# Optimization experiments

Hardware: AMD Instinct MI355X
Metric: run time of the kernel (lower is better)

Reference implementation:

```python
import jax, jax.numpy as jnp
import numpy as np

VOCAB, EMBD, H1, H2, OUT = 100000, 128, 256, 128, 1
EPS = 1e-12

def _layernorm(x, g, b):
    mu = jnp.mean(x, axis=-1, keepdims=True)
    var = jnp.mean(jnp.square(x - mu), axis=-1, keepdims=True)
    return (x - mu) * jax.lax.rsqrt(var + EPS) * g + b

def setup_inputs() -> dict:
    key = jax.random.key(0)
    ks = jax.random.split(key, 10)
    B, S = 4096, 50
    return {
        "entity_ids": jax.random.randint(ks[0], (B, S), 0, VOCAB),
        "entity_length": jax.random.randint(ks[1], (B,), 0, S + 1),
        "emb_table": jax.random.normal(ks[2], (VOCAB, EMBD), jnp.float32),
        "ln1_g": jnp.ones((EMBD,), jnp.float32),
        "ln1_b": jnp.zeros((EMBD,), jnp.float32),
        "w1": jax.random.normal(ks[3], (EMBD, H1), jnp.float32) * (1.0 / np.sqrt(EMBD)),
        "b1": jnp.zeros((H1,), jnp.float32),
        "w2": jax.random.normal(ks[4], (H1, H2), jnp.float32) * (1.0 / np.sqrt(H1)),
        "b2": jnp.zeros((H2,), jnp.float32),
        "ln2_g": jnp.ones((H2,), jnp.float32),
        "ln2_b": jnp.zeros((H2,), jnp.float32),
        "fc_w": jax.random.normal(ks[5], (H2, OUT), jnp.float32) * (1.0 / np.sqrt(H2)),
        "fc_b": jnp.zeros((OUT,), jnp.float32),
    }

def reference(entity_ids, entity_length, emb_table, ln1_g, ln1_b, w1, b1, w2, b2, ln2_g, ln2_b, fc_w, fc_b):
    # embed: [B, S, EMBD]
    x = emb_table[entity_ids]
    x = _layernorm(x, ln1_g, ln1_b)
    # MLP (dropout is identity in eval); torch GELU default is exact erf form
    x = jax.nn.gelu(x @ w1 + b1, approximate=False) @ w2 + b2  # [B, S, H2]
    # ragged max-pool over first length positions (length 0 treated as 1)
    lengths = jnp.maximum(entity_length, 1)  # [B]
    S = x.shape[1]
    mask = jnp.arange(S)[None, :] < lengths[:, None]  # [B, S]
    x = jnp.max(jnp.where(mask[:, :, None], x, -jnp.inf), axis=1)  # [B, H2]
    x = _layernorm(x, ln2_g, ln2_b)
    return (x @ fc_w + fc_b).squeeze(-1)  # [B]
```

## Files before the change

kernel.cpp:

```cpp
#include <hip/hip_runtime.h>
#include <hip/hip_bf16.h>
#include <math.h>

typedef __attribute__((ext_vector_type(8))) _Float16 half8;
typedef __attribute__((ext_vector_type(4))) _Float16 half4;
typedef __attribute__((ext_vector_type(4))) float f32x4;

#define EMBD 128
#define H1 256
#define H2 128
#define SLEN 50
#define NROWS 4096
#define MTILE 32
#define DENSE_GRID 512

#define WS_FRAGS   0
#define WS_CNT     131072
#define WS_PACKED  131200
#define WS_PARTIAL 950400

__device__ __forceinline__ float gelu_exact(float h) {
    float ah = fabsf(h);
    float d  = fmaf(0.23163845f, ah, 1.0f);
    float t;
    asm("v_rcp_f32 %0, %1" : "=v"(t) : "v"(d));
    float p = fmaf(1.061405429f, t, -1.453152027f);
    p = fmaf(p, t, 1.421413741f);
    p = fmaf(p, t, -0.284496736f);
    p = fmaf(p, t, 0.254829592f);
    p = p * t;
    float e;
    float x2 = h * h * -0.72134752f;
    asm("v_exp_f32 %0, %1" : "=v"(e) : "v"(x2));
    float er = fmaf(-p, e, 1.0f);
    return fmaf(0.5f * ah, er, 0.5f * h);
}

#define BARRIER_LDS() asm volatile("s_waitcnt lgkmcnt(0)\n\ts_barrier" ::: "memory")

__global__ __launch_bounds__(256) void setup_kernel(
    const float* __restrict__ w1, const float* __restrict__ w2,
    const int* __restrict__ ids, const int* __restrict__ lens,
    half8* __restrict__ frags, unsigned* __restrict__ packed,
    int* __restrict__ cnt, float* __restrict__ partial)
{
    int b = blockIdx.x, t = threadIdx.x;
    if (b < 32) {
        int f = b * 256 + t;
        half8 v;
        if (f < 4096) {
            int fragid = f >> 6, lane = f & 63;
            int kt = fragid >> 4, nt = fragid & 15;
            int col = nt * 16 + (lane & 15);
            int kb  = kt * 32 + (lane >> 4) * 8;
            #pragma unroll
            for (int i = 0; i < 8; ++i) v[i] = (_Float16)w1[(size_t)(kb + i) * H1 + col];
            frags[f] = v;
        } else {
            int f2 = f - 4096;
            int fragid = f2 >> 6, lane = f2 & 63;
            int kt = fragid >> 3, ntc = fragid & 7;
            int col = ntc * 16 + (lane & 15);
            int kb  = kt * 32 + (lane >> 4) * 8;
            #pragma unroll
            for (int i = 0; i < 8; ++i) v[i] = (_Float16)w2[(size_t)(kb + i) * H2 + col];
            frags[4096 + f2] = v;
        }
    } else if (b < 48) {
        int gtid = (b - 32) * 256 + t;
        int lane = t & 63;
        int len = lens[gtid]; len = len < 1 ? 1 : (len > SLEN ? SLEN : len);
        int inc = len;
        #pragma unroll
        for (int off = 1; off < 64; off <<= 1) {
            int v = __shfl_up(inc, off, 64);
            if (lane >= off) inc += v;
        }
        int wave_total = __shfl(inc, 63, 64);
        int wbase;
        if (lane == 0) wbase = atomicAdd(cnt, wave_total);
        wbase = __shfl(wbase, 0, 64);
        int base = wbase + inc - len;
        unsigned rtag = (unsigned)gtid << 17;
        for (int k = 0; k < len; ++k)
            packed[base + k] = (unsigned)ids[gtid * SLEN + k] | rtag;
    } else {
        float4 ninf = { -INFINITY, -INFINITY, -INFINITY, -INFINITY };
        float4* p4 = (float4*)partial;
        int idx = (b - 48) * 256 + t;
        for (int e = idx; e < NROWS * 64; e += 64 * 256) {
            int row = e >> 6, rem = e & 63;
            p4[row * 96 + 32 + rem] = ninf;
        }
    }
}

__global__ __launch_bounds__(512) void dense_kernel(
    const unsigned* __restrict__ packed, const int* __restrict__ cnt,
    const float* __restrict__ emb, const float* __restrict__ ln1g,
    const float* __restrict__ ln1b, const float* __restrict__ b1,
    const float* __restrict__ b2, const half8* __restrict__ wfrag,
    float* __restrict__ partial)
{
    const int tid = threadIdx.x;
    const int w  = tid >> 6;
    const int l  = tid & 63;
    const int ln = l & 15;
    const int lg = l >> 4;
    const int g32 = w * 4 + lg;

    __shared__ __align__(16) _Float16 x_lds[MTILE][EMBD + 8];
    __shared__ __align__(16) _Float16 h1_lds[MTILE][H1 + 8];
    __shared__ unsigned tok_lds[MTILE + 1];
    __shared__ __align__(16) float b1s[H1];
    __shared__ float b2s[H2];

    if (tid < H1) b1s[tid] = b1[tid];
    else if (tid < H1 + H2) b2s[tid - H1] = b2[tid - H1];

    half8 w1r[4][2];
    #pragma unroll
    for (int kt = 0; kt < 4; ++kt)
      #pragma unroll
      for (int j = 0; j < 2; ++j)
        w1r[kt][j] = wfrag[(kt * 16 + w * 2 + j) * 64 + l];
    half8 w2r[8];
    #pragma unroll
    for (int kt = 0; kt < 8; ++kt)
        w2r[kt] = wfrag[4096 + (kt * 8 + w) * 64 + l];

    float g1r[8], b1r[8];
    #pragma unroll
    for (int i = 0; i < 8; ++i) { g1r[i] = ln1g[ln * 8 + i]; b1r[i] = ln1b[ln * 8 + i]; }

    const int total = *cnt;

    int tile = blockIdx.x;
    int base = tile * MTILE;

    unsigned pkA = 0xFFFFFFFFu, tokA = 0xFFFFFFFFu;
    float4 pa0, pa1; bool vA = false;
    if (base < total) {
        if (base + g32 < total) pkA = packed[base + g32];
        if (tid <= 32) {
            int ti = (tid < 32) ? base + tid : base - 1;
            tokA = (ti >= 0 && ti < total) ? packed[ti] : 0xFFFFFFFFu;
        }
        vA = (pkA != 0xFFFFFFFFu);
        if (vA) {
            const float4* src = (const float4*)(emb + (size_t)(pkA & 0x1FFFFu) * EMBD + ln * 8);
            pa0 = src[0]; pa1 = src[1];
        }
    }

    for (; base < total; tile += (int)gridDim.x, base = tile * MTILE) {
        const int nbase = (tile + (int)gridDim.x) * MTILE;

        if (tid <= 32) tok_lds[tid] = tokA;

        unsigned pkN = 0xFFFFFFFFu, tokN = 0xFFFFFFFFu;
        if (nbase < total) {
            if (nbase + g32 < total) pkN = packed[nbase + g32];
            if (tid <= 32) {
                int ti = (tid < 32) ? nbase + tid : nbase - 1;
                tokN = (ti < total) ? packed[ti] : 0xFFFFFFFFu;
            }
        }

        {
            half8 xo;
            if (vA) {
                float v[8] = {pa0.x, pa0.y, pa0.z, pa0.w, pa1.x, pa1.y, pa1.z, pa1.w};
                float sm = 0.f, ss = 0.f;
                #pragma unroll
                for (int k = 0; k < 8; ++k) { sm += v[k]; ss += v[k] * v[k]; }
                #pragma unroll
                for (int m = 1; m < 16; m <<= 1) {
                    sm += __shfl_xor(sm, m, 64);
                    ss += __shfl_xor(ss, m, 64);
                }
                float mu  = sm * (1.f / 128.f);
                float var = ss * (1.f / 128.f) - mu * mu;
                float rs  = rsqrtf(var + 1e-12f);
                #pragma unroll
                for (int k = 0; k < 8; ++k)
                    xo[k] = (_Float16)((v[k] - mu) * rs * g1r[k] + b1r[k]);
            } else {
                #pragma unroll
                for (int k = 0; k < 8; ++k) xo[k] = (_Float16)0.f;
            }
            *(half8*)&x_lds[g32][ln * 8] = xo;
        }

        BARRIER_LDS();

        f32x4 acc[2][2];
        acc[0][0] = (f32x4){0,0,0,0}; acc[0][1] = (f32x4){0,0,0,0};
        acc[1][0] = (f32x4){0,0,0,0}; acc[1][1] = (f32x4){0,0,0,0};
        #pragma unroll
        for (int kt = 0; kt < 4; ++kt) {
            half8 xf0 = *(const half8*)&x_lds[ln][kt * 32 + lg * 8];
            half8 xf1 = *(const half8*)&x_lds[16 + ln][kt * 32 + lg * 8];
            acc[0][0] = __builtin_amdgcn_mfma_f32_16x16x32_f16(w1r[kt][0], xf0, acc[0][0], 0, 0, 0);
            acc[0][1] = __builtin_amdgcn_mfma_f32_16x16x32_f16(w1r[kt][1], xf0, acc[0][1], 0, 0, 0);
            acc[1][0] = __builtin_amdgcn_mfma_f32_16x16x32_f16(w1r[kt][0], xf1, acc[1][0], 0, 0, 0);
            acc[1][1] = __builtin_amdgcn_mfma_f32_16x16x32_f16(w1r[kt][1], xf1, acc[1][1], 0, 0, 0);
        }

        float4 pb0, pb1; bool vN = (pkN != 0xFFFFFFFFu);
        if (vN) {
            const float4* src = (const float4*)(emb + (size_t)(pkN & 0x1FFFFu) * EMBD + ln * 8);
            pb0 = src[0]; pb1 = src[1];
        }

        #pragma unroll
        for (int m = 0; m < 2; ++m)
          #pragma unroll
          for (int j = 0; j < 2; ++j) {
            f32x4 bb = *(const f32x4*)&b1s[(w * 2 + j) * 16 + lg * 4];
            half4 hv;
            #pragma unroll
            for (int g2 = 0; g2 < 4; ++g2) {
                float h = acc[m][j][g2] + bb[g2];
                hv[g2] = (_Float16)gelu_exact(h);
            }
            *(half4*)&h1_lds[m * 16 + ln][(w * 2 + j) * 16 + lg * 4] = hv;
          }

        int rowj = 0x7FFF, rowp = 0x7FFF;
        if (l < 32) {
            rowj = (int)(tok_lds[l] >> 17);
            rowp = (l == 0) ? (int)(tok_lds[32] >> 17) : (int)(tok_lds[l - 1] >> 17);
        }
        const int prevrow = (int)(tok_lds[32] >> 17);
        bool st = (l < 32) && ((l == 0) || (rowj != rowp));
        unsigned mask = (unsigned)__ballot(st);
        const float b2v = b2s[w * 16 + ln];

        BARRIER_LDS();

        f32x4 acc2[2];
        acc2[0] = (f32x4){0,0,0,0}; acc2[1] = (f32x4){0,0,0,0};
        #pragma unroll
        for (int kt = 0; kt < 8; ++kt) {
            half8 a0 = *(const half8*)&h1_lds[ln][kt * 32 + lg * 8];
            half8 a1 = *(const half8*)&h1_lds[16 + ln][kt * 32 + lg * 8];
            acc2[0] = __builtin_amdgcn_mfma_f32_16x16x32_f16(a0, w2r[kt], acc2[0], 0, 0, 0);
            acc2[1] = __builtin_amdgcn_mfma_f32_16x16x32_f16(a1, w2r[kt], acc2[1], 0, 0, 0);
        }
        float val[2][4];
        #pragma unroll
        for (int m = 0; m < 2; ++m)
          #pragma unroll
          for (int g2 = 0; g2 < 4; ++g2)
            val[m][g2] = acc2[m][g2] + b2v;

        {
            int s0 = 0;
            while (s0 < 32) {
                int s1;
                if (s0 >= 31) s1 = 32;
                else {
                    unsigned m2 = mask >> (s0 + 1);
                    s1 = m2 ? (s0 + __ffs(m2)) : 32;
                }
                int row = __shfl(rowj, s0, 64);
                if (row < NROWS) {
                    float mx = -INFINITY;
                    #pragma unroll
                    for (int m = 0; m < 2; ++m)
                      #pragma unroll
                      for (int g2 = 0; g2 < 4; ++g2) {
                        int tt = m * 16 + lg * 4 + g2;
                        if (tt >= s0 && tt < s1) mx = fmaxf(mx, val[m][g2]);
                      }
                    mx = fmaxf(mx, __shfl_xor(mx, 16, 64));
                    mx = fmaxf(mx, __shfl_xor(mx, 32, 64));
                    int side = (s0 == 0 && row == prevrow) ? 1 + (tile & 1) : 0;
                    if (l < 16)
                        partial[(size_t)row * 384 + side * 128 + w * 16 + l] = mx;
                }
                s0 = s1;
            }
        }

        pkA = pkN; tokA = tokN; vA = vN;
        if (vN) { pa0 = pb0; pa1 = pb1; }
    }
}

__global__ __launch_bounds__(256) void head_kernel(
    const float* __restrict__ partial, const float* __restrict__ ln2g,
    const float* __restrict__ ln2b, const float* __restrict__ fcw,
    const float* __restrict__ fcb, float* __restrict__ out)
{
    int w = threadIdx.x >> 6, l = threadIdx.x & 63;
    int r = blockIdx.x * 4 + w;
    const float* pr = partial + (size_t)r * 384;
    float v0 = fmaxf(fmaxf(pr[l],      pr[128 + l]),      pr[256 + l]);
    float v1 = fmaxf(fmaxf(pr[64 + l], pr[128 + 64 + l]), pr[256 + 64 + l]);
    float g2a = ln2g[l], g2c = ln2g[l + 64];
    float b2a = ln2b[l], b2c = ln2b[l + 64];
    float fwa = fcw[l],  fwc = fcw[l + 64];
    float s = v0 + v1, ss = v0 * v0 + v1 * v1;
    #pragma unroll
    for (int m = 1; m < 64; m <<= 1) {
        s  += __shfl_xor(s,  m, 64);
        ss += __shfl_xor(ss, m, 64);
    }
    float mu  = s * (1.f / 128.f);
    float var = ss * (1.f / 128.f) - mu * mu;
    float rs  = rsqrtf(var + 1e-12f);
    float n0 = (v0 - mu) * rs * g2a + b2a;
    float n1 = (v1 - mu) * rs * g2c + b2c;
    float dot = n0 * fwa + n1 * fwc;
    #pragma unroll
    for (int m = 1; m < 64; m <<= 1) dot += __shfl_xor(dot, m, 64);
    if (l == 0) out[r] = dot + fcb[0];
}

extern "C" void kernel_launch(void* const* d_in, const int* in_sizes, int n_in,
                              void* d_out, int out_size, void* d_ws, size_t ws_size,
                              hipStream_t stream) {
    const int*   ids  = (const int*)d_in[0];
    const int*   lens = (const int*)d_in[1];
    const float* emb  = (const float*)d_in[2];
    const float* ln1g = (const float*)d_in[3];
    const float* ln1b = (const float*)d_in[4];
    const float* w1   = (const float*)d_in[5];
    const float* b1   = (const float*)d_in[6];
    const float* w2   = (const float*)d_in[7];
    const float* b2   = (const float*)d_in[8];
    const float* ln2g = (const float*)d_in[9];
    const float* ln2b = (const float*)d_in[10];
    const float* fcw  = (const float*)d_in[11];
    const float* fcb  = (const float*)d_in[12];
    float* out = (float*)d_out;

    char* ws = (char*)d_ws;
    half8*    frags   = (half8*)(ws + WS_FRAGS);
    int*      cnt     = (int*)(ws + WS_CNT);
    unsigned* packed  = (unsigned*)(ws + WS_PACKED);
    float*    partial = (float*)(ws + WS_PARTIAL);

    hipMemsetAsync(cnt, 0, sizeof(int), stream);
    hipLaunchKernelGGL(setup_kernel, dim3(112), dim3(256), 0, stream,
                       w1, w2, ids, lens, frags, packed, cnt, partial);
    hipLaunchKernelGGL(dense_kernel, dim3(DENSE_GRID), dim3(512), 0, stream,
                       packed, cnt, emb, ln1g, ln1b, b1, b2, frags, partial);
    hipLaunchKernelGGL(head_kernel, dim3(1024), dim3(256), 0, stream,
                       partial, ln2g, ln2b, fcw, fcb, out);
}
```

Before: 72.58 us.

## Parallelize row packing per wave, drop partial -inf init, double dense grid

Setup now packs each row's token ids with one wave per row, using a per-row atomic and lane-parallel stores instead of a serial per-thread loop after a wave prefix scan. It records each row's start offset, so the head kernel can work out which tiles a row spans and read only the partial slots that were written. That removes the -inf initialization pass over the partial buffer. The dense grid is doubled to 1024 blocks. Per-row atomics raise contention on the single counter, and row order in the packed buffer becomes nondeterministic.

```diff
diff --git a/kernel.cpp b/kernel.cpp
--- a/kernel.cpp
+++ b/kernel.cpp
@@ -12,12 +12,13 @@
 #define SLEN 50
 #define NROWS 4096
 #define MTILE 32
-#define DENSE_GRID 512
-
-#define WS_FRAGS   0
-#define WS_CNT     131072
-#define WS_PACKED  131200
-#define WS_PARTIAL 950400
+#define DENSE_GRID 1024
+
+#define WS_FRAGS    0
+#define WS_CNT      131072
+#define WS_ROWSTART 131200
+#define WS_PACKED   147584
+#define WS_PARTIAL  966784
 
 __device__ __forceinline__ float gelu_exact(float h) {
     float ah = fabsf(h);
@@ -38,15 +39,15 @@
 
 #define BARRIER_LDS() asm volatile("s_waitcnt lgkmcnt(0)\n\ts_barrier" ::: "memory")
 
-__global__ __launch_bounds__(256) void setup_kernel(
+__global__ __launch_bounds__(512) void setup_kernel(
     const float* __restrict__ w1, const float* __restrict__ w2,
     const int* __restrict__ ids, const int* __restrict__ lens,
     half8* __restrict__ frags, unsigned* __restrict__ packed,
-    int* __restrict__ cnt, float* __restrict__ partial)
+    int* __restrict__ cnt, int* __restrict__ rowstart)
 {
     int b = blockIdx.x, t = threadIdx.x;
-    if (b < 32) {
-        int f = b * 256 + t;
+    if (b < 16) {
+        int f = b * 512 + t;
         half8 v;
         if (f < 4096) {
             int fragid = f >> 6, lane = f & 63;
@@ -66,32 +67,16 @@
             for (int i = 0; i < 8; ++i) v[i] = (_Float16)w2[(size_t)(kb + i) * H2 + col];
             frags[4096 + f2] = v;
         }
-    } else if (b < 48) {
-        int gtid = (b - 32) * 256 + t;
+    } else {
+        int r    = (b - 16) * 8 + (t >> 6);
         int lane = t & 63;
-        int len = lens[gtid]; len = len < 1 ? 1 : (len > SLEN ? SLEN : len);
-        int inc = len;
-        #pragma unroll
-        for (int off = 1; off < 64; off <<= 1) {
-            int v = __shfl_up(inc, off, 64);
-            if (lane >= off) inc += v;
-        }
-        int wave_total = __shfl(inc, 63, 64);
-        int wbase;
-        if (lane == 0) wbase = atomicAdd(cnt, wave_total);
-        wbase = __shfl(wbase, 0, 64);
-        int base = wbase + inc - len;
-        unsigned rtag = (unsigned)gtid << 17;
-        for (int k = 0; k < len; ++k)
-            packed[base + k] = (unsigned)ids[gtid * SLEN + k] | rtag;
-    } else {
-        float4 ninf = { -INFINITY, -INFINITY, -INFINITY, -INFINITY };
-        float4* p4 = (float4*)partial;
-        int idx = (b - 48) * 256 + t;
-        for (int e = idx; e < NROWS * 64; e += 64 * 256) {
-            int row = e >> 6, rem = e & 63;
-            p4[row * 96 + 32 + rem] = ninf;
-        }
+        int len = lens[r]; len = len < 1 ? 1 : (len > SLEN ? SLEN : len);
+        int base;
+        if (lane == 0) base = atomicAdd(cnt, len);
+        base = __shfl(base, 0, 64);
+        if (lane == 0) rowstart[r] = base;
+        if (lane < len)
+            packed[base + lane] = (unsigned)ids[r * SLEN + lane] | ((unsigned)r << 17);
     }
 }
 
@@ -290,15 +275,31 @@
 }
 
 __global__ __launch_bounds__(256) void head_kernel(
-    const float* __restrict__ partial, const float* __restrict__ ln2g,
+    const float* __restrict__ partial, const int* __restrict__ rowstart,
+    const int* __restrict__ lens, const float* __restrict__ ln2g,
     const float* __restrict__ ln2b, const float* __restrict__ fcw,
     const float* __restrict__ fcb, float* __restrict__ out)
 {
     int w = threadIdx.x >> 6, l = threadIdx.x & 63;
     int r = blockIdx.x * 4 + w;
     const float* pr = partial + (size_t)r * 384;
-    float v0 = fmaxf(fmaxf(pr[l],      pr[128 + l]),      pr[256 + l]);
-    float v1 = fmaxf(fmaxf(pr[64 + l], pr[128 + 64 + l]), pr[256 + 64 + l]);
+
+    int start = rowstart[r];
+    int len = lens[r]; len = len < 1 ? 1 : (len > SLEN ? SLEN : len);
+    int tf = start >> 5, tl = (start + len - 1) >> 5;
+
+    float v0 = pr[l], v1 = pr[64 + l];
+    if (tl > tf) {
+        int side = 1 + ((tf + 1) & 1);
+        v0 = fmaxf(v0, pr[side * 128 + l]);
+        v1 = fmaxf(v1, pr[side * 128 + 64 + l]);
+    }
+    if (tl > tf + 1) {
+        int side = 1 + ((tf + 2) & 1);
+        v0 = fmaxf(v0, pr[side * 128 + l]);
+        v1 = fmaxf(v1, pr[side * 128 + 64 + l]);
+    }
+
     float g2a = ln2g[l], g2c = ln2g[l + 64];
     float b2a = ln2b[l], b2c = ln2b[l + 64];
     float fwa = fcw[l],  fwc = fcw[l + 64];
@@ -338,16 +339,17 @@
     float* out = (float*)d_out;
 
     char* ws = (char*)d_ws;
-    half8*    frags   = (half8*)(ws + WS_FRAGS);
-    int*      cnt     = (int*)(ws + WS_CNT);
-    unsigned* packed  = (unsigned*)(ws + WS_PACKED);
-    float*    partial = (float*)(ws + WS_PARTIAL);
+    half8*    frags    = (half8*)(ws + WS_FRAGS);
+    int*      cnt      = (int*)(ws + WS_CNT);
+    int*      rowstart = (int*)(ws + WS_ROWSTART);
+    unsigned* packed   = (unsigned*)(ws + WS_PACKED);
+    float*    partial  = (float*)(ws + WS_PARTIAL);
 
     hipMemsetAsync(cnt, 0, sizeof(int), stream);
-    hipLaunchKernelGGL(setup_kernel, dim3(112), dim3(256), 0, stream,
-                       w1, w2, ids, lens, frags, packed, cnt, partial);
+    hipLaunchKernelGGL(setup_kernel, dim3(528), dim3(512), 0, stream,
+                       w1, w2, ids, lens, frags, packed, cnt, rowstart);
     hipLaunchKernelGGL(dense_kernel, dim3(DENSE_GRID), dim3(512), 0, stream,
                        packed, cnt, emb, ln1g, ln1b, b1, b2, frags, partial);
     hipLaunchKernelGGL(head_kernel, dim3(1024), dim3(256), 0, stream,
-                       partial, ln2g, ln2b, fcw, fcb, out);
-}
+                       partial, rowstart, lens, ln2g, ln2b, fcw, fcb, out);
+}
```

Result: slower. 113.3 us (+56.1%).
